# Kernel optimization log

Measured on AMD Instinct MI355X. Metric: run time of the kernel, lower is better.

Reference implementation:

```python
import jax, jax.numpy as jnp
import numpy as np

CAPACITY_FACTOR = 1.25


def setup_inputs() -> dict:
    key = jax.random.key(0)
    k1, k2, k3, k4 = jax.random.split(key, 4)
    B, T, H = 2, 2048, 1024
    E, F = 8, 2048
    x = jax.random.normal(k1, (B, T, H), dtype=jnp.float32)
    Wr = jax.random.normal(k2, (H, E), dtype=jnp.float32) * 0.02
    W1 = jax.random.normal(k3, (E, H, 2 * F), dtype=jnp.float32) * 0.02
    W2 = jax.random.normal(k4, (E, F, H), dtype=jnp.float32) * 0.02
    return {"x": x, "Wr": Wr, "W1": W1, "W2": W2}


def _moe_forward(x, Wr, W1, W2):
    B, T, H = x.shape
    E = Wr.shape[1]
    N = B * T
    cap = max(1, int(CAPACITY_FACTOR * (N * 2 / E)))  # static (shape-derived)

    flat_x = x.reshape(N, H)
    logits = flat_x @ Wr                      # [N, E] (train=False: no noise)
    gate = jax.nn.softmax(logits, axis=-1)
    top2_val, top2_idx = jax.lax.top_k(gate, 2)   # [N,2]

    # --- capacity bookkeeping, matching the torch sequential fill order ---
    e0, e1 = top2_idx[:, 0], top2_idx[:, 1]
    oh0 = jax.nn.one_hot(e0, E, dtype=jnp.int32)  # [N,E]
    oh1 = jax.nn.one_hot(e1, E, dtype=jnp.int32)
    # rank of each token within its expert's k=0 queue (flattened token order)
    pos0 = jnp.take_along_axis(jnp.cumsum(oh0, axis=0), top2_idx[:, :1], axis=1)[:, 0] - 1
    count0 = oh0.sum(axis=0)                      # tokens routed top-1 per expert
    used0 = jnp.minimum(count0, cap)              # slots consumed in k=0 pass
    keep0 = pos0 < cap
    # k=1 pass starts after the slots used by k=0
    pos1 = jnp.take_along_axis(jnp.cumsum(oh1, axis=0), top2_idx[:, 1:2], axis=1)[:, 0] - 1
    pos1 = pos1 + used0[e1]
    keep1 = pos1 < cap

    dummy = E * cap  # drop slot
    slot0 = jnp.where(keep0, e0 * cap + pos0, dummy)
    slot1 = jnp.where(keep1, e1 * cap + pos1, dummy)

    # --- dispatch: [E*cap+1, H] buffer (last row is the drop slot) ---
    buf = jnp.zeros((E * cap + 1, H), dtype=x.dtype)
    buf = buf.at[slot0].set(flat_x).at[slot1].set(flat_x)
    xe = buf[: E * cap].reshape(E, cap, H)

    # --- grouped expert FFN (SwiGLU) ---
    h = jnp.einsum("ech,ehf->ecf", xe, W1)        # [E, cap, 2F]
    a, b = jnp.split(h, 2, axis=-1)
    act = jax.nn.silu(a) * b                      # [E, cap, F]
    out = jnp.einsum("ecf,efh->ech", act, W2)     # [E, cap, H]
    out_flat = out.reshape(E * cap, H)

    # --- combine: gather back per token, weighted by gate values ---
    g0 = out_flat[jnp.where(keep0, slot0, 0)] * keep0[:, None]
    g1 = out_flat[jnp.where(keep1, slot1, 0)] * keep1[:, None]
    y = g0 * top2_val[:, 0:1] + g1 * top2_val[:, 1:2]
    y = y.reshape(B, T, H)

    # --- balance loss ---
    me = 1e-9
    prob_per_expert = gate.mean(axis=0)                 # == mean over (B,T)
    used1 = (oh1 * keep1[:, None].astype(jnp.int32)).sum(axis=0)
    used = (used0 + used1).astype(gate.dtype)
    frac_used = jnp.maximum(used, me) / (N * 2 + me)
    balance_loss = (prob_per_expert * frac_used).sum() * E
    return y, balance_loss


def reference(x, Wr, W1, W2):
    return _moe_forward(x, Wr, W1, W2)
```

## Files before the change

### kernel.cpp

```cpp
#include <hip/hip_runtime.h>
#include <cstdint>

#define E_    8
#define H_    1024
#define F_    2048
#define NTOK  4096
#define CAP   1280
#define ECAP  (E_*CAP)

typedef unsigned short u16;
typedef __attribute__((ext_vector_type(8))) short bf16x8;
typedef __attribute__((ext_vector_type(4))) float f32x4;
typedef __attribute__((ext_vector_type(4))) unsigned short u16x4;
typedef __attribute__((ext_vector_type(8))) unsigned short u16x8;

__device__ __forceinline__ u16 f2bf(float f) {
  union { float f; uint32_t u; } v; v.f = f;
  uint32_t r = v.u + 0x7fffu + ((v.u >> 16) & 1u);
  return (u16)(r >> 16);
}

__device__ __forceinline__ void gld16(const void* gsrc, void* ldst) {
  auto g = reinterpret_cast<const __attribute__((address_space(1))) uint32_t*>(
      reinterpret_cast<uintptr_t>(gsrc));
  auto l = reinterpret_cast<__attribute__((address_space(3))) uint32_t*>(
      reinterpret_cast<uintptr_t>(ldst));
  __builtin_amdgcn_global_load_lds(g, l, 16, 0, 0);
}

__device__ __forceinline__ int swz(int row, int chunk) {
  return row * 64 + ((chunk ^ (row & 7)) * 8);
}

__global__ __launch_bounds__(256) void prep_kernel(const float* __restrict__ W1,
                                                   const float* __restrict__ W2,
                                                   u16* __restrict__ W1T,
                                                   u16* __restrict__ W2T,
                                                   const float* __restrict__ x,
                                                   const float* __restrict__ Wr,
                                                   int* __restrict__ e0o, int* __restrict__ e1o,
                                                   float* __restrict__ v0o, float* __restrict__ v1o,
                                                   float* __restrict__ partial) {
  int b = blockIdx.x;
  if (b < 12288) {
    __shared__ u16 tile[64 * 70];
    const float* in; u16* outp; int R, C, rt, ct;
    if (b < 8192) {
      int slab = b >> 10, t = b & 1023;
      rt = t >> 6; ct = t & 63;
      R = H_; C = 2 * F_;
      in = W1 + (size_t)slab * R * C;
      outp = W1T + (size_t)slab * R * C;
    } else {
      int bb = b - 8192;
      int slab = bb >> 9, t = bb & 511;
      rt = t >> 4; ct = t & 15;
      R = F_; C = H_;
      in = W2 + (size_t)slab * R * C;
      outp = W2T + (size_t)slab * R * C;
    }
    int r0 = rt * 64, c0 = ct * 64;
    int t = threadIdx.x;
    int col4 = t & 15, row = t >> 4;
#pragma unroll
    for (int i = 0; i < 4; i++) {
      int r = row + 16 * i;
      float4 v = *(const float4*)(in + (size_t)(r0 + r) * C + c0 + col4 * 4);
      u16x4 q;
      q.x = f2bf(v.x); q.y = f2bf(v.y); q.z = f2bf(v.z); q.w = f2bf(v.w);
      *(u16x4*)&tile[r * 70 + col4 * 4] = q;
    }
    __syncthreads();
    int lane8 = t & 7, cc = t >> 3;
#pragma unroll
    for (int j = 0; j < 2; j++) {
      int c = cc + 32 * j;
      u16x8 q;
#pragma unroll
      for (int k = 0; k < 8; k++) q[k] = tile[(lane8 * 8 + k) * 70 + c];
      *(u16x8*)(outp + (size_t)(c0 + c) * R + r0 + lane8 * 8) = q;
    }
  } else {
    int blk = b - 12288;
    int w = threadIdx.x >> 6, l = threadIdx.x & 63;
    int t = blk * 4 + w;
    const float* xr = x + (size_t)t * H_;
    float acc[8] = {0.f,0.f,0.f,0.f,0.f,0.f,0.f,0.f};
#pragma unroll
    for (int it = 0; it < 16; ++it) {
      int h = it * 64 + l;
      float xv = xr[h];
      const float4* wr = (const float4*)(Wr + h * 8);
      float4 wa = wr[0], wb = wr[1];
      acc[0] += xv * wa.x; acc[1] += xv * wa.y; acc[2] += xv * wa.z; acc[3] += xv * wa.w;
      acc[4] += xv * wb.x; acc[5] += xv * wb.y; acc[6] += xv * wb.z; acc[7] += xv * wb.w;
    }
#pragma unroll
    for (int e = 0; e < 8; ++e)
#pragma unroll
      for (int off = 32; off; off >>= 1)
        acc[e] += __shfl_xor(acc[e], off);

    __shared__ float pg[4][8];
    if (l == 0) {
      float mx = acc[0];
#pragma unroll
      for (int e = 1; e < 8; ++e) mx = fmaxf(mx, acc[e]);
      float g[8], s = 0.f;
#pragma unroll
      for (int e = 0; e < 8; ++e) { g[e] = __expf(acc[e] - mx); s += g[e]; }
      float inv = 1.f / s;
#pragma unroll
      for (int e = 0; e < 8; ++e) g[e] *= inv;
      int b0 = 0; float m0 = g[0];
#pragma unroll
      for (int e = 1; e < 8; ++e) if (g[e] > m0) { m0 = g[e]; b0 = e; }
      int b1 = -1; float m1 = -1.f;
#pragma unroll
      for (int e = 0; e < 8; ++e) if (e != b0 && g[e] > m1) { m1 = g[e]; b1 = e; }
      e0o[t] = b0; e1o[t] = b1; v0o[t] = m0; v1o[t] = m1;
#pragma unroll
      for (int e = 0; e < 8; ++e) pg[w][e] = g[e];
    }
    __syncthreads();
    if (threadIdx.x < 8) {
      int e = threadIdx.x;
      partial[blk * 8 + e] = pg[0][e] + pg[1][e] + pg[2][e] + pg[3][e];
    }
  }
}

__global__ __launch_bounds__(256) void scan_kernel(const int* __restrict__ e0i, const int* __restrict__ e1i,
                                                   const float* __restrict__ partial,
                                                   int* __restrict__ slot0, int* __restrict__ slot1,
                                                   int* __restrict__ used_out,
                                                   float* __restrict__ bl_out) {
  __shared__ int c0[256][8], c1[256][8];
  __shared__ float gs[256][8];
  __shared__ int used0_s[8], tot1_s[8];
  int tid = threadIdx.x;

  int le0[16], le1[16];
  int lc0[8] = {0,0,0,0,0,0,0,0}, lc1[8] = {0,0,0,0,0,0,0,0};
  for (int i = 0; i < 16; ++i) {
    int t = tid * 16 + i;
    le0[i] = e0i[t]; le1[i] = e1i[t];
    lc0[le0[i]]++; lc1[le1[i]]++;
  }
#pragma unroll
  for (int e = 0; e < 8; ++e) { c0[tid][e] = lc0[e]; c1[tid][e] = lc1[e]; }

  float g[8] = {0.f,0.f,0.f,0.f,0.f,0.f,0.f,0.f};
  for (int rr = 0; rr < 4; ++rr)
#pragma unroll
    for (int e = 0; e < 8; ++e) g[e] += partial[(tid + rr * 256) * 8 + e];
#pragma unroll
  for (int e = 0; e < 8; ++e) gs[tid][e] = g[e];
  __syncthreads();

  for (int d = 1; d < 256; d <<= 1) {
    int t0[8], t1[8];
    bool a = (tid >= d);
    if (a) {
#pragma unroll
      for (int e = 0; e < 8; ++e) { t0[e] = c0[tid - d][e]; t1[e] = c1[tid - d][e]; }
    }
    __syncthreads();
    if (a) {
#pragma unroll
      for (int e = 0; e < 8; ++e) { c0[tid][e] += t0[e]; c1[tid][e] += t1[e]; }
    }
    __syncthreads();
  }
  for (int s = 128; s > 0; s >>= 1) {
    if (tid < s)
#pragma unroll
      for (int e = 0; e < 8; ++e) gs[tid][e] += gs[tid + s][e];
    __syncthreads();
  }
  if (tid < 8) {
    int e = tid;
    int u0 = min(c0[255][e], CAP);
    int t1 = c1[255][e];
    used0_s[e] = u0;
    tot1_s[e] = t1;
    used_out[e] = u0 + min(t1, max(0, CAP - u0));
  }
  __syncthreads();

  int ex0[8], ex1[8];
#pragma unroll
  for (int e = 0; e < 8; ++e) { ex0[e] = c0[tid][e] - lc0[e]; ex1[e] = c1[tid][e] - lc1[e]; }
  int r0c[8] = {0,0,0,0,0,0,0,0}, r1c[8] = {0,0,0,0,0,0,0,0};
  for (int i = 0; i < 16; ++i) {
    int t = tid * 16 + i;
    int e = le0[i];
    int pos = ex0[e] + r0c[e]; r0c[e]++;
    slot0[t] = (pos < CAP) ? (e * CAP + pos) : -1;
    e = le1[i];
    pos = ex1[e] + r1c[e] + used0_s[e]; r1c[e]++;
    slot1[t] = (pos < CAP) ? (e * CAP + pos) : -1;
  }

  if (tid == 0) {
    float bl = 0.f;
    for (int e = 0; e < 8; ++e) {
      int u1 = min(tot1_s[e], max(0, CAP - used0_s[e]));
      float used = (float)(used0_s[e] + u1);
      float fu = fmaxf(used, 1e-9f) / (8192.f + 1e-9f);
      bl += (gs[0][e] / (float)NTOK) * fu;
    }
    bl_out[0] = bl * 8.f;
  }
}

__global__ __launch_bounds__(256) void scatter_kernel(const float* __restrict__ x,
                                                      const int* __restrict__ slot0,
                                                      const int* __restrict__ slot1,
                                                      u16* __restrict__ xe) {
  int t = blockIdx.x, tid = threadIdx.x;
  float4 vv = *(const float4*)(x + (size_t)t * H_ + tid * 4);
  u16x4 b;
  b.x = f2bf(vv.x); b.y = f2bf(vv.y); b.z = f2bf(vv.z); b.w = f2bf(vv.w);
  int s0 = slot0[t], s1 = slot1[t];
  if (s0 >= 0) *(u16x4*)(xe + (size_t)s0 * H_ + tid * 4) = b;
  if (s1 >= 0) *(u16x4*)(xe + (size_t)s1 * H_ + tid * 4) = b;
}

__global__ __launch_bounds__(256, 2) void gemm1_kernel(const u16* __restrict__ xe,
                                                       const u16* __restrict__ W1T,
                                                       const int* __restrict__ used_tot,
                                                       u16* __restrict__ act) {
  const int mbase = blockIdx.y * 128;
  const int e = mbase / 1280;
  if (mbase - e * 1280 >= used_tot[e]) return;

  __shared__ u16 As[128 * 64];
  __shared__ u16 Bsa[64 * 64];
  __shared__ u16 Bsb[64 * 64];
  const int tid = threadIdx.x;
  const int w = tid >> 6, l = tid & 63;
  const int wm = w & 1, wn = w >> 1;
  const int nbase = blockIdx.x * 64;
  const u16* Ap = xe + (size_t)mbase * H_;
  const u16* Ba = W1T + (size_t)e * 4096 * H_ + (size_t)nbase * H_;
  const u16* Bb = Ba + (size_t)F_ * H_;
  const int lrow = l >> 3;
  const int lcol = (((l & 7) ^ lrow) * 8);

  f32x4 acca[4][2] = {};
  f32x4 accb[4][2] = {};

  for (int kt = 0; kt < 16; ++kt) {
    int k0 = kt * 64;
#pragma unroll
    for (int r = 0; r < 4; ++r) {
      int row0 = w * 32 + r * 8;
      gld16(Ap + (size_t)(row0 + lrow) * H_ + k0 + lcol, &As[row0 * 64]);
    }
#pragma unroll
    for (int r = 0; r < 2; ++r) {
      int row0 = w * 16 + r * 8;
      gld16(Ba + (size_t)(row0 + lrow) * H_ + k0 + lcol, &Bsa[row0 * 64]);
      gld16(Bb + (size_t)(row0 + lrow) * H_ + k0 + lcol, &Bsb[row0 * 64]);
    }
    __syncthreads();
#pragma unroll
    for (int kk = 0; kk < 64; kk += 32) {
      const int ck = (kk >> 3) + (l >> 4);
      bf16x8 af[4], ba[2], bb[2];
#pragma unroll
      for (int i = 0; i < 4; ++i)
        af[i] = *(const bf16x8*)&As[swz(wm * 64 + i * 16 + (l & 15), ck)];
#pragma unroll
      for (int j = 0; j < 2; ++j) {
        ba[j] = *(const bf16x8*)&Bsa[swz(wn * 32 + j * 16 + (l & 15), ck)];
        bb[j] = *(const bf16x8*)&Bsb[swz(wn * 32 + j * 16 + (l & 15), ck)];
      }
#pragma unroll
      for (int i = 0; i < 4; ++i)
#pragma unroll
        for (int j = 0; j < 2; ++j) {
          acca[i][j] = __builtin_amdgcn_mfma_f32_16x16x32_bf16(af[i], ba[j], acca[i][j], 0, 0, 0);
          accb[i][j] = __builtin_amdgcn_mfma_f32_16x16x32_bf16(af[i], bb[j], accb[i][j], 0, 0, 0);
        }
    }
    __syncthreads();
  }
#pragma unroll
  for (int i = 0; i < 4; ++i)
#pragma unroll
    for (int j = 0; j < 2; ++j)
#pragma unroll
      for (int r = 0; r < 4; ++r) {
        int m = mbase + wm * 64 + i * 16 + (l >> 4) * 4 + r;
        int f = nbase + wn * 32 + j * 16 + (l & 15);
        float a = acca[i][j][r];
        float b = accb[i][j][r];
        float s = a / (1.f + __expf(-a));
        act[(size_t)m * F_ + f] = f2bf(s * b);
      }
}

__global__ __launch_bounds__(256, 2) void gemm2_kernel(const u16* __restrict__ act,
                                                       const u16* __restrict__ W2T,
                                                       const int* __restrict__ used_tot,
                                                       float* __restrict__ outb) {
  const int mbase = blockIdx.y * 128;
  const int e = mbase / 1280;
  if (mbase - e * 1280 >= used_tot[e]) return;

  __shared__ u16 As[128 * 64];
  __shared__ u16 Bs[128 * 64];
  const int tid = threadIdx.x;
  const int w = tid >> 6, l = tid & 63;
  const int wm = w & 1, wn = w >> 1;
  const int nbase = blockIdx.x * 128;
  const u16* Ap = act + (size_t)mbase * F_;
  const u16* Bp = W2T + (size_t)e * H_ * F_ + (size_t)nbase * F_;
  const int lrow = l >> 3;
  const int lcol = (((l & 7) ^ lrow) * 8);

  f32x4 acc[4][4] = {};

  for (int kt = 0; kt < 32; ++kt) {
    int k0 = kt * 64;
#pragma unroll
    for (int r = 0; r < 4; ++r) {
      int row0 = w * 32 + r * 8;
      gld16(Ap + (size_t)(row0 + lrow) * F_ + k0 + lcol, &As[row0 * 64]);
      gld16(Bp + (size_t)(row0 + lrow) * F_ + k0 + lcol, &Bs[row0 * 64]);
    }
    __syncthreads();
#pragma unroll
    for (int kk = 0; kk < 64; kk += 32) {
      const int ck = (kk >> 3) + (l >> 4);
      bf16x8 af[4], bf[4];
#pragma unroll
      for (int i = 0; i < 4; ++i)
        af[i] = *(const bf16x8*)&As[swz(wm * 64 + i * 16 + (l & 15), ck)];
#pragma unroll
      for (int j = 0; j < 4; ++j)
        bf[j] = *(const bf16x8*)&Bs[swz(wn * 64 + j * 16 + (l & 15), ck)];
#pragma unroll
      for (int i = 0; i < 4; ++i)
#pragma unroll
        for (int j = 0; j < 4; ++j)
          acc[i][j] = __builtin_amdgcn_mfma_f32_16x16x32_bf16(af[i], bf[j], acc[i][j], 0, 0, 0);
    }
    __syncthreads();
  }
#pragma unroll
  for (int i = 0; i < 4; ++i)
#pragma unroll
    for (int j = 0; j < 4; ++j)
#pragma unroll
      for (int r = 0; r < 4; ++r) {
        int m = mbase + wm * 64 + i * 16 + (l >> 4) * 4 + r;
        int n = nbase + wn * 64 + j * 16 + (l & 15);
        outb[(size_t)m * H_ + n] = acc[i][j][r];
      }
}

__global__ __launch_bounds__(256) void combine_kernel(const float* __restrict__ outb,
                                                      const int* __restrict__ slot0,
                                                      const int* __restrict__ slot1,
                                                      const float* __restrict__ v0,
                                                      const float* __restrict__ v1,
                                                      float* __restrict__ y) {
  int t = blockIdx.x, tid = threadIdx.x;
  int s0 = slot0[t], s1 = slot1[t];
  float w0 = v0[t], w1 = v1[t];
  float4 r; r.x = 0.f; r.y = 0.f; r.z = 0.f; r.w = 0.f;
  if (s0 >= 0) {
    float4 a = *(const float4*)(outb + (size_t)s0 * H_ + tid * 4);
    r.x += w0 * a.x; r.y += w0 * a.y; r.z += w0 * a.z; r.w += w0 * a.w;
  }
  if (s1 >= 0) {
    float4 a = *(const float4*)(outb + (size_t)s1 * H_ + tid * 4);
    r.x += w1 * a.x; r.y += w1 * a.y; r.z += w1 * a.z; r.w += w1 * a.w;
  }
  *(float4*)(y + (size_t)t * H_ + tid * 4) = r;
}

#define OFF_W1T   ((size_t)0)
#define OFF_W2T   ((size_t)67108864)
#define OFF_XE    ((size_t)100663296)
#define OFF_ACT   ((size_t)121634816)
#define OFF_OUTB  ((size_t)163577856)
#define OFF_SLOT0 ((size_t)205520896)
#define OFF_SLOT1 ((size_t)205537280)
#define OFF_V0    ((size_t)205553664)
#define OFF_V1    ((size_t)205570048)
#define OFF_E0    ((size_t)205586432)
#define OFF_E1    ((size_t)205602816)
#define OFF_PART  ((size_t)205619200)
#define OFF_USED  ((size_t)205651968)

extern "C" void kernel_launch(void* const* d_in, const int* in_sizes, int n_in,
                              void* d_out, int out_size, void* d_ws, size_t ws_size,
                              hipStream_t stream) {
  const float* x  = (const float*)d_in[0];
  const float* Wr = (const float*)d_in[1];
  const float* W1 = (const float*)d_in[2];
  const float* W2 = (const float*)d_in[3];
  float* out = (float*)d_out;

  uint8_t* ws = (uint8_t*)d_ws;
  u16*   W1T   = (u16*)(ws + OFF_W1T);
  u16*   W2T   = (u16*)(ws + OFF_W2T);
  u16*   xe    = (u16*)(ws + OFF_XE);
  u16*   act   = (u16*)(ws + OFF_ACT);
  float* outb  = (float*)(ws + OFF_OUTB);
  int*   slot0 = (int*)(ws + OFF_SLOT0);
  int*   slot1 = (int*)(ws + OFF_SLOT1);
  float* v0    = (float*)(ws + OFF_V0);
  float* v1    = (float*)(ws + OFF_V1);
  int*   e0    = (int*)(ws + OFF_E0);
  int*   e1    = (int*)(ws + OFF_E1);
  float* part  = (float*)(ws + OFF_PART);
  int*   used  = (int*)(ws + OFF_USED);

  prep_kernel<<<13312, 256, 0, stream>>>(W1, W2, W1T, W2T, x, Wr, e0, e1, v0, v1, part);

  scan_kernel<<<1, 256, 0, stream>>>(e0, e1, part, slot0, slot1, used, out + (size_t)NTOK * H_);
  scatter_kernel<<<NTOK, 256, 0, stream>>>(x, slot0, slot1, xe);

  gemm1_kernel<<<dim3(F_ / 64, ECAP / 128), 256, 0, stream>>>(xe, W1T, used, act);
  gemm2_kernel<<<dim3(H_ / 128, ECAP / 128), 256, 0, stream>>>(act, W2T, used, outb);

  combine_kernel<<<NTOK, 256, 0, stream>>>(outb, slot0, slot1, v0, v1, out);
}
```

Baseline: 222.4 us.

## Store transposed bf16 weights in contiguous 64x64 tiles for GEMM loads

The prep kernel now writes W1 and W2 as contiguous 64x64 bf16 tiles, indexed by expert, output tile and k tile, in place of row-major transposed matrices. The GEMM kernels load each B tile from one contiguous 8KB block, so each load touches fewer DRAM pages and TLB entries. The transpose staging in shared memory switches to a padded float tile with narrower 8-byte stores, which may cost a little in the prep kernel.

```diff
diff --git a/kernel.cpp b/kernel.cpp
--- a/kernel.cpp
+++ b/kernel.cpp
@@ -12,7 +12,6 @@
 typedef __attribute__((ext_vector_type(8))) short bf16x8;
 typedef __attribute__((ext_vector_type(4))) float f32x4;
 typedef __attribute__((ext_vector_type(4))) unsigned short u16x4;
-typedef __attribute__((ext_vector_type(8))) unsigned short u16x8;
 
 __device__ __forceinline__ u16 f2bf(float f) {
   union { float f; uint32_t u; } v; v.f = f;
@@ -30,6 +29,13 @@
 
 __device__ __forceinline__ int swz(int row, int chunk) {
   return row * 64 + ((chunk ^ (row & 7)) * 8);
+}
+
+__device__ __forceinline__ size_t w1_tile(int e, int nt, int kt) {
+  return (((size_t)e * 64 + nt) * 16 + kt) * 4096;
+}
+__device__ __forceinline__ size_t w2_tile(int e, int nt, int kt) {
+  return (((size_t)e * 16 + nt) * 32 + kt) * 4096;
 }
 
 __global__ __launch_bounds__(256) void prep_kernel(const float* __restrict__ W1,
@@ -43,42 +49,45 @@
                                                    float* __restrict__ partial) {
   int b = blockIdx.x;
   if (b < 12288) {
-    __shared__ u16 tile[64 * 70];
-    const float* in; u16* outp; int R, C, rt, ct;
+    __shared__ float tile[64][65];
+    const float* in; u16* outp; int C, r0, c0;
     if (b < 8192) {
       int slab = b >> 10, t = b & 1023;
-      rt = t >> 6; ct = t & 63;
-      R = H_; C = 2 * F_;
-      in = W1 + (size_t)slab * R * C;
-      outp = W1T + (size_t)slab * R * C;
+      int nt = t & 63, kt = t >> 6;
+      C = 2 * F_;
+      r0 = kt * 64; c0 = nt * 64;
+      in = W1 + (size_t)slab * H_ * C;
+      outp = W1T + w1_tile(slab, nt, kt);
     } else {
       int bb = b - 8192;
       int slab = bb >> 9, t = bb & 511;
-      rt = t >> 4; ct = t & 15;
-      R = F_; C = H_;
-      in = W2 + (size_t)slab * R * C;
-      outp = W2T + (size_t)slab * R * C;
-    }
-    int r0 = rt * 64, c0 = ct * 64;
+      int nt = t & 15, kt = t >> 4;
+      C = H_;
+      r0 = kt * 64; c0 = nt * 64;
+      in = W2 + (size_t)slab * F_ * C;
+      outp = W2T + w2_tile(slab, nt, kt);
+    }
     int t = threadIdx.x;
-    int col4 = t & 15, row = t >> 4;
+    int tx = t & 15, ty = t >> 4;
 #pragma unroll
     for (int i = 0; i < 4; i++) {
-      int r = row + 16 * i;
-      float4 v = *(const float4*)(in + (size_t)(r0 + r) * C + c0 + col4 * 4);
+      int r = ty + 16 * i;
+      float4 v = *(const float4*)(in + (size_t)(r0 + r) * C + c0 + tx * 4);
+      tile[r][tx * 4 + 0] = v.x;
+      tile[r][tx * 4 + 1] = v.y;
+      tile[r][tx * 4 + 2] = v.z;
+      tile[r][tx * 4 + 3] = v.w;
+    }
+    __syncthreads();
+#pragma unroll
+    for (int i = 0; i < 4; i++) {
+      int c = ty + 16 * i;
       u16x4 q;
-      q.x = f2bf(v.x); q.y = f2bf(v.y); q.z = f2bf(v.z); q.w = f2bf(v.w);
-      *(u16x4*)&tile[r * 70 + col4 * 4] = q;
-    }
-    __syncthreads();
-    int lane8 = t & 7, cc = t >> 3;
-#pragma unroll
-    for (int j = 0; j < 2; j++) {
-      int c = cc + 32 * j;
-      u16x8 q;
-#pragma unroll
-      for (int k = 0; k < 8; k++) q[k] = tile[(lane8 * 8 + k) * 70 + c];
-      *(u16x8*)(outp + (size_t)(c0 + c) * R + r0 + lane8 * 8) = q;
+      q.x = f2bf(tile[tx * 4 + 0][c]);
+      q.y = f2bf(tile[tx * 4 + 1][c]);
+      q.z = f2bf(tile[tx * 4 + 2][c]);
+      q.w = f2bf(tile[tx * 4 + 3][c]);
+      *(u16x4*)(outp + c * 64 + tx * 4) = q;
     }
   } else {
     int blk = b - 12288;
@@ -241,10 +250,9 @@
   const int tid = threadIdx.x;
   const int w = tid >> 6, l = tid & 63;
   const int wm = w & 1, wn = w >> 1;
-  const int nbase = blockIdx.x * 64;
+  const int bx = blockIdx.x;
+  const int nbase = bx * 64;
   const u16* Ap = xe + (size_t)mbase * H_;
-  const u16* Ba = W1T + (size_t)e * 4096 * H_ + (size_t)nbase * H_;
-  const u16* Bb = Ba + (size_t)F_ * H_;
   const int lrow = l >> 3;
   const int lcol = (((l & 7) ^ lrow) * 8);
 
@@ -253,6 +261,8 @@
 
   for (int kt = 0; kt < 16; ++kt) {
     int k0 = kt * 64;
+    const u16* BaT = W1T + w1_tile(e, bx, kt);
+    const u16* BbT = W1T + w1_tile(e, bx + 32, kt);
 #pragma unroll
     for (int r = 0; r < 4; ++r) {
       int row0 = w * 32 + r * 8;
@@ -261,8 +271,8 @@
 #pragma unroll
     for (int r = 0; r < 2; ++r) {
       int row0 = w * 16 + r * 8;
-      gld16(Ba + (size_t)(row0 + lrow) * H_ + k0 + lcol, &Bsa[row0 * 64]);
-      gld16(Bb + (size_t)(row0 + lrow) * H_ + k0 + lcol, &Bsb[row0 * 64]);
+      gld16(BaT + (row0 + lrow) * 64 + lcol, &Bsa[row0 * 64]);
+      gld16(BbT + (row0 + lrow) * 64 + lcol, &Bsb[row0 * 64]);
     }
     __syncthreads();
 #pragma unroll
@@ -315,9 +325,9 @@
   const int tid = threadIdx.x;
   const int w = tid >> 6, l = tid & 63;
   const int wm = w & 1, wn = w >> 1;
-  const int nbase = blockIdx.x * 128;
+  const int bx = blockIdx.x;
+  const int nbase = bx * 128;
   const u16* Ap = act + (size_t)mbase * F_;
-  const u16* Bp = W2T + (size_t)e * H_ * F_ + (size_t)nbase * F_;
   const int lrow = l >> 3;
   const int lcol = (((l & 7) ^ lrow) * 8);
 
@@ -329,7 +339,9 @@
     for (int r = 0; r < 4; ++r) {
       int row0 = w * 32 + r * 8;
       gld16(Ap + (size_t)(row0 + lrow) * F_ + k0 + lcol, &As[row0 * 64]);
-      gld16(Bp + (size_t)(row0 + lrow) * F_ + k0 + lcol, &Bs[row0 * 64]);
+      int tsel = row0 >> 6;
+      const u16* BT = W2T + w2_tile(e, bx * 2 + tsel, kt);
+      gld16(BT + ((row0 & 63) + lrow) * 64 + lcol, &Bs[row0 * 64]);
     }
     __syncthreads();
 #pragma unroll
```

Result: no change. 222.6 us (+0.1%).
